# Kernel optimization log

Hardware: AMD Instinct MI355X
Metric: run time of the kernel (lower is better)

Reference implementation:

```python
import jax, jax.numpy as jnp
import numpy as np

B, S, D, H = 2, 2048, 1024, 16
DEPTH = D // H
NEG = -1e9

def setup_inputs() -> dict:
    key = jax.random.key(0)
    k = jax.random.split(key, 4)
    return {
        "token_inputs": jax.random.normal(k[0], (B, S, D), dtype=jnp.float32),
        "mask": jnp.zeros((B, 1, 1, S), dtype=jnp.float32),
        "W_qkv": jax.random.normal(k[1], (D, 3 * D), dtype=jnp.float32) * 0.02,
        "b_qkv": jnp.zeros((3 * D,), dtype=jnp.float32),
        "W_out": jax.random.normal(k[2], (D, D), dtype=jnp.float32) * 0.02,
        "b_out": jnp.zeros((D,), dtype=jnp.float32),
    }

def reference(token_inputs, mask, W_qkv, b_qkv, W_out, b_out):
    # fused QKV projection
    qkv = token_inputs @ W_qkv + b_qkv                       # [B,S,3D]
    q, k, v = jnp.split(qkv, 3, axis=-1)                     # [B,S,D] each
    # split heads -> [B,H,S,depth]
    split = lambda x: x.reshape(B, S, H, DEPTH).transpose(0, 2, 1, 3)
    q, k, v = split(q), split(k), split(v)
    # causal additive mask: 0 on/below diagonal, -1e9 above
    causal = (1.0 - jnp.tril(jnp.ones((S, S), dtype=jnp.float32))) * NEG
    full_mask = mask + causal                                # [B,1,S,S]
    # scaled dot-product attention
    scores = jnp.einsum('bhqd,bhkd->bhqk', q, k) / jnp.sqrt(jnp.float32(DEPTH))
    scores = scores + full_mask
    attn = jax.nn.softmax(scores, axis=-1)                   # [B,H,S,S]
    ctx = jnp.einsum('bhqk,bhkd->bhqd', attn, v)             # [B,H,S,depth]
    # merge heads and final projection
    ctx = ctx.transpose(0, 2, 1, 3).reshape(B, S, D)
    return ctx @ W_out + b_out
```

## Files before the change

kernel.cpp:

```cpp
#include <hip/hip_runtime.h>
#include <hip/hip_bf16.h>

#define B_ 2
#define S_ 2048
#define D_ 1024
#define H_ 16
#define DEPTH_ 64

typedef __attribute__((ext_vector_type(4))) float f32x4;
typedef __attribute__((ext_vector_type(16))) float f32x16;
typedef __attribute__((ext_vector_type(8))) short bf16x8;
typedef const __attribute__((address_space(1))) unsigned int gu32;
typedef __attribute__((address_space(3))) unsigned int lu32;

__device__ __forceinline__ void gload_lds16(const void* g, void* l) {
  __builtin_amdgcn_global_load_lds((gu32*)g, (lu32*)l, 16, 0, 0);
}

__device__ __forceinline__ short f2bf(float f) {
  union { float f; unsigned u; } v; v.f = f;
  return (short)((v.u + 0x7FFFu + ((v.u >> 16) & 1u)) >> 16);
}
__device__ __forceinline__ unsigned pk2(float lo, float hi) {
  unsigned r;
  asm("v_cvt_pk_bf16_f32 %0, %1, %2" : "=v"(r) : "v"(lo), "v"(hi));
  return r;
}

__global__ __launch_bounds__(256) void cast_kernel(const float* __restrict__ in,
                                                   short* __restrict__ out, int n4) {
  int i = blockIdx.x * 256 + threadIdx.x;
  if (i < n4) {
    const float4 v = reinterpret_cast<const float4*>(in)[i];
    short2 a, b;
    *reinterpret_cast<unsigned*>(&a) = pk2(v.x, v.y);
    *reinterpret_cast<unsigned*>(&b) = pk2(v.z, v.w);
    reinterpret_cast<short4*>(out)[i] = make_short4(a.x, a.y, b.x, b.y);
  }
}

__global__ __launch_bounds__(256) void transpose_cast_kernel(const float* __restrict__ W,
                                                             short* __restrict__ WT,
                                                             int K, int N) {
  __shared__ short tile[32][33];
  int n0 = blockIdx.x * 32, k0 = blockIdx.y * 32;
  int tx = threadIdx.x, ty = threadIdx.y;
#pragma unroll
  for (int j = 0; j < 4; ++j)
    tile[ty + 8 * j][tx] = f2bf(W[(size_t)(k0 + ty + 8 * j) * N + n0 + tx]);
  __syncthreads();
#pragma unroll
  for (int j = 0; j < 4; ++j)
    WT[(size_t)(n0 + ty + 8 * j) * K + k0 + tx] = tile[tx][ty + 8 * j];
}

template <int EPI, int BM>
__global__ __launch_bounds__(512) void gemm_bt_kernel(
    const short* __restrict__ A, const short* __restrict__ BT,
    const float* __restrict__ bias,
    short* __restrict__ Qh, short* __restrict__ Kh, short* __restrict__ VTt,
    float* __restrict__ Out, int M, int N, int K) {
  constexpr int MI = BM / 64;
  constexpr int ASZ = BM * 32;
  constexpr int BSZ = 128 * 32;
  __shared__ short smem[2 * ASZ + 2 * BSZ];
  const int bm = blockIdx.y * BM, bn = blockIdx.x * 128;
  const int tid = threadIdx.x;
  const int w = tid >> 6, lane = tid & 63;
  const int wr = w >> 1, wc = w & 1;
  const int lr = lane & 15, lg = lane >> 4;
  const int s_r = lane >> 2, s_c = (lane & 3) * 8;
  f32x4 acc[MI][4] = {};
  const int nk = K >> 5;

  auto stage = [&](int buf, int kt) {
    short* Asb = smem + (buf ? ASZ : 0);
    short* Bsb = smem + 2 * ASZ + (buf ? BSZ : 0);
    if (BM == 128 || w < 4)
      gload_lds16(&A[(size_t)(bm + 16 * w + s_r) * K + kt * 32 + s_c], &Asb[16 * w * 32]);
    gload_lds16(&BT[(size_t)(bn + 16 * w + s_r) * K + kt * 32 + s_c], &Bsb[16 * w * 32]);
  };

  stage(0, 0);
  __syncthreads();
  int cur = 0;
  for (int kt = 0; kt < nk; ++kt) {
    if (kt + 1 < nk) stage(cur ^ 1, kt + 1);
    const short* Asb = smem + (cur ? ASZ : 0);
    const short* Bsb = smem + 2 * ASZ + (cur ? BSZ : 0);
    bf16x8 af[MI], bfr[4];
#pragma unroll
    for (int mi = 0; mi < MI; ++mi)
      af[mi] = *reinterpret_cast<const bf16x8*>(&Asb[((BM / 4) * wr + 16 * mi + lr) * 32 + 8 * lg]);
#pragma unroll
    for (int ni = 0; ni < 4; ++ni)
      bfr[ni] = *reinterpret_cast<const bf16x8*>(&Bsb[(64 * wc + 16 * ni + lr) * 32 + 8 * lg]);
#pragma unroll
    for (int mi = 0; mi < MI; ++mi)
#pragma unroll
      for (int ni = 0; ni < 4; ++ni)
        acc[mi][ni] = __builtin_amdgcn_mfma_f32_16x16x32_bf16(af[mi], bfr[ni], acc[mi][ni], 0, 0, 0);
    __syncthreads();
    cur ^= 1;
  }

  if constexpr (EPI == 0) {
    if (bn >= 2 * D_) {
      __syncthreads();
      short* vt = smem;
#pragma unroll
      for (int mi = 0; mi < MI; ++mi)
#pragma unroll
        for (int ni = 0; ni < 4; ++ni)
#pragma unroll
          for (int r = 0; r < 4; r += 2) {
            int row_local = (BM / 4) * wr + 16 * mi + 4 * lg + r;
            int col_local = 64 * wc + 16 * ni + lr;
            float bv = bias[bn + col_local];
            unsigned u = pk2(acc[mi][ni][r] + bv, acc[mi][ni][r + 1] + bv);
            int rsw = row_local ^ ((col_local & 7) << 3);
            *reinterpret_cast<unsigned*>(&vt[col_local * 128 + rsw]) = u;
          }
      __syncthreads();
      const int b = bm >> 11, sbase = bm & (S_ - 1);
#pragma unroll
      for (int p = 0; p < 4; ++p) {
        int slot = 512 * p + tid;
        int vrow = slot >> 4, seg = slot & 15;
        int dd_col = bn - 2 * D_ + vrow;
        int hh = dd_col >> 6, dd = dd_col & 63;
        int csw = (seg * 8) ^ ((vrow & 7) << 3);
        short* dst = &VTt[((size_t)(b * H_ + hh) * DEPTH_ + dd) * S_ + sbase + seg * 8];
        *reinterpret_cast<bf16x8*>(dst) = *reinterpret_cast<const bf16x8*>(&vt[vrow * 128 + csw]);
      }
    } else {
      constexpr float SCQ = 0.125f * 1.44269504f;
#pragma unroll
      for (int mi = 0; mi < MI; ++mi)
#pragma unroll
        for (int ni = 0; ni < 4; ++ni)
#pragma unroll
          for (int r = 0; r < 4; ++r) {
            int row = bm + (BM / 4) * wr + 16 * mi + 4 * lg + r;
            int col = bn + 64 * wc + 16 * ni + lr;
            float v = acc[mi][ni][r] + bias[col];
            int b = row >> 11, s = row & (S_ - 1);
            int which = col >> 10, cm = col & (D_ - 1);
            int hh = cm >> 6, dd = cm & 63;
            size_t bh = (size_t)(b * H_ + hh);
            if (which == 0) Qh[(bh * S_ + s) * DEPTH_ + dd] = f2bf(v * SCQ);
            else            Kh[(bh * S_ + s) * DEPTH_ + dd] = f2bf(v);
          }
    }
  } else {
#pragma unroll
    for (int mi = 0; mi < MI; ++mi)
#pragma unroll
      for (int ni = 0; ni < 4; ++ni)
#pragma unroll
        for (int r = 0; r < 4; ++r) {
          int row = bm + (BM / 4) * wr + 16 * mi + 4 * lg + r;
          int col = bn + 64 * wc + 16 * ni + lr;
          Out[(size_t)row * N + col] = acc[mi][ni][r] + bias[col];
        }
  }
}

__global__ __launch_bounds__(256, 4) void attn_kernel(
    const short* __restrict__ Qh, const short* __restrict__ Kh,
    const short* __restrict__ VTt, const float* __restrict__ mask,
    short* __restrict__ ctx) {
  constexpr float LOG2E = 1.44269504f;
  __shared__ short smem[16384];
  const int bid = blockIdx.x;
  const int j = bid >> 5, g = j & 7, rr = j >> 3;
  const int qt = (rr == 0) ? 31 - g : (rr == 1) ? 16 + g : (rr == 2) ? 15 - g : g;
  const int bh = bid & 31;
  const int b = bh >> 4, h = bh & 15;
  const short* Qp = Qh + (size_t)bh * S_ * DEPTH_;
  const short* Kp = Kh + (size_t)bh * S_ * DEPTH_;
  const short* Vp = VTt + (size_t)bh * DEPTH_ * S_;
  const int tid = threadIdx.x;
  const int w = tid >> 6, lane = tid & 63;
  const int sw = w & 1, ch = w >> 1;
  const int lq = lane & 31, hi = lane >> 5;
  const int q0w = qt * 64 + sw * 32;
  const int scs = 8 * ((lane & 7) ^ ((lane >> 3) & 7));
  const int srw = lane >> 3;
  short* Ksc = smem + ch * 8192;
  short* Vsc = Ksc + 4096;

  bf16x8 qf[4];
#pragma unroll
  for (int ksd = 0; ksd < 4; ++ksd)
    qf[ksd] = *reinterpret_cast<const bf16x8*>(&Qp[(size_t)(q0w + lq) * DEPTH_ + 16 * ksd + 8 * hi]);

  bf16x8 ones = {};
  if (hi == 0) ones[0] = (short)0x3F80;

  f32x16 acc0 = {}, acc1 = {};
  float l_run = 0.f;

  const int nt = qt + 1;
  const int nh = (nt + 1) >> 1;
  for (int i = 0; i < nh; ++i) {
    const int kt = ch ? (nh + i) : i;
    const bool valid = kt < nt;
    const int k0 = kt * 64;
    __syncthreads();
    if (valid) {
#pragma unroll
      for (int jj = 0; jj < 4; ++jj) {
        const int brow = sw * 32 + jj * 8;
        gload_lds16(&Kp[(size_t)(k0 + brow + srw) * DEPTH_ + scs], &Ksc[brow * 64]);
        gload_lds16(&Vp[(size_t)(brow + srw) * S_ + k0 + scs], &Vsc[brow * 64]);
      }
    }
    __syncthreads();
    if (!valid) continue;

    f32x16 sc[2] = {{}, {}};
#pragma unroll
    for (int h2 = 0; h2 < 2; ++h2) {
#pragma unroll
      for (int ksd = 0; ksd < 4; ++ksd) {
        const int row = h2 * 32 + lq;
        const int col = (16 * ksd + 8 * hi) ^ ((row & 7) * 8);
        bf16x8 kf = *reinterpret_cast<const bf16x8*>(&Ksc[row * 64 + col]);
        sc[h2] = __builtin_amdgcn_mfma_f32_32x32x16_bf16(kf, qf[ksd], sc[h2], 0, 0, 0);
      }
      float mv = mask[(size_t)b * S_ + k0 + h2 * 32 + lq];
      bf16x8 maf = {};
      if (hi == 0) maf[0] = f2bf(LOG2E * mv);
      sc[h2] = __builtin_amdgcn_mfma_f32_32x32x16_bf16(maf, ones, sc[h2], 0, 0, 0);
    }
    if (kt == nt - 1) {
      const int qg = q0w + lq;
#pragma unroll
      for (int h2 = 0; h2 < 2; ++h2)
#pragma unroll
        for (int r = 0; r < 16; ++r) {
          int kvg = k0 + (r & 3) + 8 * (r >> 2) + 4 * hi + 32 * h2;
          if (kvg > qg) sc[h2][r] = -1e30f;
        }
    }
#pragma unroll
    for (int h2 = 0; h2 < 2; ++h2)
#pragma unroll
      for (int r = 0; r < 16; ++r) sc[h2][r] = exp2f(sc[h2][r]);
    float s8[8];
#pragma unroll
    for (int r = 0; r < 8; ++r) s8[r] = (sc[0][r] + sc[0][r + 8]) + (sc[1][r] + sc[1][r + 8]);
#pragma unroll
    for (int r = 0; r < 4; ++r) s8[r] = s8[r] + s8[r + 4];
    float su = (s8[0] + s8[1]) + (s8[2] + s8[3]);
    su += __shfl_xor(su, 32);
    l_run += su;

#pragma unroll
    for (int h2 = 0; h2 < 2; ++h2) {
#pragma unroll
      for (int ks = 0; ks < 2; ++ks) {
        const int rb = 8 * ks;
        unsigned a = pk2(sc[h2][rb + 0], sc[h2][rb + 1]);
        unsigned bq = pk2(sc[h2][rb + 2], sc[h2][rb + 3]);
        unsigned c = pk2(sc[h2][rb + 4], sc[h2][rb + 5]);
        unsigned d = pk2(sc[h2][rb + 6], sc[h2][rb + 7]);
        unsigned sa = __shfl_xor((int)a, 32), sb = __shfl_xor((int)bq, 32);
        unsigned sx = __shfl_xor((int)c, 32), sy = __shfl_xor((int)d, 32);
        union { unsigned u[4]; bf16x8 v; } pf;
        pf.u[0] = hi ? sx : a;
        pf.u[1] = hi ? sy : bq;
        pf.u[2] = hi ? c : sa;
        pf.u[3] = hi ? d : sb;
#pragma unroll
        for (int dh = 0; dh < 2; ++dh) {
          const int row = dh * 32 + lq;
          const int col = (32 * h2 + 16 * ks + 8 * hi) ^ ((row & 7) * 8);
          bf16x8 vf = *reinterpret_cast<const bf16x8*>(&Vsc[row * 64 + col]);
          if (dh == 0) acc0 = __builtin_amdgcn_mfma_f32_32x32x16_bf16(vf, pf.v, acc0, 0, 0, 0);
          else         acc1 = __builtin_amdgcn_mfma_f32_32x32x16_bf16(vf, pf.v, acc1, 0, 0, 0);
        }
      }
    }
  }

  __syncthreads();
  float* F  = (float*)smem;
  float* ML = (float*)(smem + 8192);
  short* ob = smem + 8704;
  if (ch == 1) {
    float* dst = F + ((size_t)sw * 64 + lane) * 32;
#pragma unroll
    for (int r = 0; r < 16; ++r) { dst[r] = acc0[r]; dst[16 + r] = acc1[r]; }
    ML[sw * 64 + lane] = l_run;
  }
  __syncthreads();
  if (ch == 0) {
    const float* src = F + ((size_t)sw * 64 + lane) * 32;
    const float rl = 1.f / (l_run + ML[sw * 64 + lane]);
#pragma unroll
    for (int r = 0; r < 16; ++r) {
      acc0[r] = (acc0[r] + src[r]) * rl;
      acc1[r] = (acc1[r] + src[16 + r]) * rl;
    }
#pragma unroll
    for (int dh = 0; dh < 2; ++dh) {
      const f32x16& Aa = dh ? acc1 : acc0;
#pragma unroll
      for (int gg = 0; gg < 4; ++gg)
#pragma unroll
        for (int p = 0; p < 2; ++p) {
          int r0 = 4 * gg + 2 * p;
          int d0 = 2 * p + 8 * gg + 4 * hi + 32 * dh;
          unsigned u = pk2(Aa[r0], Aa[r0 + 1]);
          *reinterpret_cast<unsigned*>(&ob[(sw * 32 + lq) * 72 + d0]) = u;
        }
    }
  }
  __syncthreads();
  {
    const int row = tid >> 2, seg = tid & 3;
    short* dst = ctx + ((size_t)b * S_ + qt * 64 + row) * D_ + h * 64 + seg * 16;
    const short* srcp = &ob[row * 72 + seg * 16];
    *reinterpret_cast<bf16x8*>(dst) = *reinterpret_cast<const bf16x8*>(srcp);
    *reinterpret_cast<bf16x8*>(dst + 8) = *reinterpret_cast<const bf16x8*>(srcp + 8);
  }
}

extern "C" void kernel_launch(void* const* d_in, const int* in_sizes, int n_in,
                              void* d_out, int out_size, void* d_ws, size_t ws_size,
                              hipStream_t stream) {
  const float* X    = (const float*)d_in[0];
  const float* mask = (const float*)d_in[1];
  const float* Wqkv = (const float*)d_in[2];
  const float* bqkv = (const float*)d_in[3];
  const float* Wout = (const float*)d_in[4];
  const float* bout = (const float*)d_in[5];
  float* Out = (float*)d_out;

  short* ws    = (short*)d_ws;
  short* Xb    = ws;
  short* WqkvT = Xb + (size_t)4096 * 1024;
  short* WoutT = WqkvT + (size_t)3072 * 1024;
  short* Qh    = WoutT + (size_t)1024 * 1024;
  short* Kh    = Qh + (size_t)B_ * H_ * S_ * DEPTH_;
  short* VTt   = Kh + (size_t)B_ * H_ * S_ * DEPTH_;
  short* ctx   = VTt + (size_t)B_ * H_ * S_ * DEPTH_;

  cast_kernel<<<4096, 256, 0, stream>>>(X, Xb, (4096 * 1024) / 4);
  transpose_cast_kernel<<<dim3(96, 32), dim3(32, 8), 0, stream>>>(Wqkv, WqkvT, 1024, 3072);
  transpose_cast_kernel<<<dim3(32, 32), dim3(32, 8), 0, stream>>>(Wout, WoutT, 1024, 1024);
  gemm_bt_kernel<0, 128><<<dim3(24, 32), 512, 0, stream>>>(Xb, WqkvT, bqkv, Qh, Kh, VTt, nullptr,
                                                           4096, 3072, 1024);
  attn_kernel<<<1024, 256, 0, stream>>>(Qh, Kh, VTt, mask, ctx);
  gemm_bt_kernel<1, 64><<<dim3(8, 64), 512, 0, stream>>>(ctx, WoutT, bout, nullptr, nullptr, nullptr,
                                                         Out, 4096, 1024, 1024);
}
```

Before: 115.6 us.

## Register-prefetch K/V tiles in attention and use explicit vmcnt waits in GEMM

After: 164.6 us. 1.42x slower.

```diff
diff --git a/kernel.cpp b/kernel.cpp
--- a/kernel.cpp
+++ b/kernel.cpp
@@ -26,6 +26,13 @@
   asm("v_cvt_pk_bf16_f32 %0, %1, %2" : "=v"(r) : "v"(lo), "v"(hi));
   return r;
 }
+#define BARRIER_RAW() do {                      \
+  __builtin_amdgcn_sched_barrier(0);            \
+  asm volatile("" ::: "memory");                \
+  __builtin_amdgcn_s_barrier();                 \
+  asm volatile("" ::: "memory");                \
+  __builtin_amdgcn_sched_barrier(0);            \
+} while (0)
 
 __global__ __launch_bounds__(256) void cast_kernel(const float* __restrict__ in,
                                                    short* __restrict__ out, int n4) {
@@ -82,10 +89,18 @@
   };
 
   stage(0, 0);
-  __syncthreads();
+  asm volatile("s_waitcnt vmcnt(0)" ::: "memory");
+  BARRIER_RAW();
   int cur = 0;
   for (int kt = 0; kt < nk; ++kt) {
-    if (kt + 1 < nk) stage(cur ^ 1, kt + 1);
+    if (kt + 1 < nk) {
+      stage(cur ^ 1, kt + 1);
+      if (BM == 128 || w < 4) asm volatile("s_waitcnt vmcnt(2)" ::: "memory");
+      else                    asm volatile("s_waitcnt vmcnt(1)" ::: "memory");
+    } else {
+      asm volatile("s_waitcnt vmcnt(0)" ::: "memory");
+    }
+    BARRIER_RAW();
     const short* Asb = smem + (cur ? ASZ : 0);
     const short* Bsb = smem + 2 * ASZ + (cur ? BSZ : 0);
     bf16x8 af[MI], bfr[4];
@@ -100,7 +115,7 @@
 #pragma unroll
       for (int ni = 0; ni < 4; ++ni)
         acc[mi][ni] = __builtin_amdgcn_mfma_f32_16x16x32_bf16(af[mi], bfr[ni], acc[mi][ni], 0, 0, 0);
-    __syncthreads();
+    BARRIER_RAW();
     cur ^= 1;
   }
 
@@ -171,7 +186,8 @@
     const short* __restrict__ VTt, const float* __restrict__ mask,
     short* __restrict__ ctx) {
   constexpr float LOG2E = 1.44269504f;
-  __shared__ short smem[16384];
+  constexpr int LK = 72;
+  __shared__ short smem[2 * 2 * 64 * LK];
   const int bid = blockIdx.x;
   const int j = bid >> 5, g = j & 7, rr = j >> 3;
   const int qt = (rr == 0) ? 31 - g : (rr == 1) ? 16 + g : (rr == 2) ? 15 - g : g;
@@ -185,10 +201,29 @@
   const int sw = w & 1, ch = w >> 1;
   const int lq = lane & 31, hi = lane >> 5;
   const int q0w = qt * 64 + sw * 32;
-  const int scs = 8 * ((lane & 7) ^ ((lane >> 3) & 7));
-  const int srw = lane >> 3;
-  short* Ksc = smem + ch * 8192;
-  short* Vsc = Ksc + 4096;
+  const int lrow = lane >> 3;
+  const int lcol8 = (lane & 7) * 8;
+  short* Ksc = smem + ch * (2 * 64 * LK);
+  short* Vsc = Ksc + 64 * LK;
+
+  bf16x8 tk[4], tv[4];
+  auto loadKV = [&](int kt) {
+    const int k0 = kt * 64;
+#pragma unroll
+    for (int jj = 0; jj < 4; ++jj) {
+      const int row = sw * 32 + jj * 8 + lrow;
+      tk[jj] = *reinterpret_cast<const bf16x8*>(&Kp[(size_t)(k0 + row) * DEPTH_ + lcol8]);
+      tv[jj] = *reinterpret_cast<const bf16x8*>(&Vp[(size_t)row * S_ + k0 + lcol8]);
+    }
+  };
+  auto writeKV = [&]() {
+#pragma unroll
+    for (int jj = 0; jj < 4; ++jj) {
+      const int row = sw * 32 + jj * 8 + lrow;
+      *reinterpret_cast<bf16x8*>(&Ksc[row * LK + lcol8]) = tk[jj];
+      *reinterpret_cast<bf16x8*>(&Vsc[row * LK + lcol8]) = tv[jj];
+    }
+  };
 
   bf16x8 qf[4];
 #pragma unroll
@@ -203,92 +238,90 @@
 
   const int nt = qt + 1;
   const int nh = (nt + 1) >> 1;
+  {
+    const int kt0 = ch ? nh : 0;
+    if (kt0 < nt) { loadKV(kt0); writeKV(); }
+  }
+  __syncthreads();
   for (int i = 0; i < nh; ++i) {
     const int kt = ch ? (nh + i) : i;
     const bool valid = kt < nt;
-    const int k0 = kt * 64;
-    __syncthreads();
+    const bool nvalid = (i + 1 < nh) && (kt + 1 < nt);
+    if (nvalid) loadKV(kt + 1);
     if (valid) {
-#pragma unroll
-      for (int jj = 0; jj < 4; ++jj) {
-        const int brow = sw * 32 + jj * 8;
-        gload_lds16(&Kp[(size_t)(k0 + brow + srw) * DEPTH_ + scs], &Ksc[brow * 64]);
-        gload_lds16(&Vp[(size_t)(brow + srw) * S_ + k0 + scs], &Vsc[brow * 64]);
+      const int k0 = kt * 64;
+      f32x16 sc[2] = {{}, {}};
+#pragma unroll
+      for (int h2 = 0; h2 < 2; ++h2) {
+#pragma unroll
+        for (int ksd = 0; ksd < 4; ++ksd) {
+          const int row = h2 * 32 + lq;
+          bf16x8 kf = *reinterpret_cast<const bf16x8*>(&Ksc[row * LK + 16 * ksd + 8 * hi]);
+          sc[h2] = __builtin_amdgcn_mfma_f32_32x32x16_bf16(kf, qf[ksd], sc[h2], 0, 0, 0);
+        }
+        float mv = mask[(size_t)b * S_ + k0 + h2 * 32 + lq];
+        bf16x8 maf = {};
+        if (hi == 0) maf[0] = f2bf(LOG2E * mv);
+        sc[h2] = __builtin_amdgcn_mfma_f32_32x32x16_bf16(maf, ones, sc[h2], 0, 0, 0);
       }
-    }
-    __syncthreads();
-    if (!valid) continue;
-
-    f32x16 sc[2] = {{}, {}};
-#pragma unroll
-    for (int h2 = 0; h2 < 2; ++h2) {
-#pragma unroll
-      for (int ksd = 0; ksd < 4; ++ksd) {
-        const int row = h2 * 32 + lq;
-        const int col = (16 * ksd + 8 * hi) ^ ((row & 7) * 8);
-        bf16x8 kf = *reinterpret_cast<const bf16x8*>(&Ksc[row * 64 + col]);
-        sc[h2] = __builtin_amdgcn_mfma_f32_32x32x16_bf16(kf, qf[ksd], sc[h2], 0, 0, 0);
+      if (kt == nt - 1) {
+        const int qg = q0w + lq;
+#pragma unroll
+        for (int h2 = 0; h2 < 2; ++h2)
+#pragma unroll
+          for (int r = 0; r < 16; ++r) {
+            int kvg = k0 + (r & 3) + 8 * (r >> 2) + 4 * hi + 32 * h2;
+            if (kvg > qg) sc[h2][r] = -1e30f;
+          }
       }
-      float mv = mask[(size_t)b * S_ + k0 + h2 * 32 + lq];
-      bf16x8 maf = {};
-      if (hi == 0) maf[0] = f2bf(LOG2E * mv);
-      sc[h2] = __builtin_amdgcn_mfma_f32_32x32x16_bf16(maf, ones, sc[h2], 0, 0, 0);
-    }
-    if (kt == nt - 1) {
-      const int qg = q0w + lq;
 #pragma unroll
       for (int h2 = 0; h2 < 2; ++h2)
 #pragma unroll
-        for (int r = 0; r < 16; ++r) {
-          int kvg = k0 + (r & 3) + 8 * (r >> 2) + 4 * hi + 32 * h2;
-          if (kvg > qg) sc[h2][r] = -1e30f;
-        }
-    }
-#pragma unroll
-    for (int h2 = 0; h2 < 2; ++h2)
-#pragma unroll
-      for (int r = 0; r < 16; ++r) sc[h2][r] = exp2f(sc[h2][r]);
-    float s8[8];
-#pragma unroll
-    for (int r = 0; r < 8; ++r) s8[r] = (sc[0][r] + sc[0][r + 8]) + (sc[1][r] + sc[1][r + 8]);
-#pragma unroll
-    for (int r = 0; r < 4; ++r) s8[r] = s8[r] + s8[r + 4];
-    float su = (s8[0] + s8[1]) + (s8[2] + s8[3]);
-    su += __shfl_xor(su, 32);
-    l_run += su;
-
-#pragma unroll
-    for (int h2 = 0; h2 < 2; ++h2) {
-#pragma unroll
-      for (int ks = 0; ks < 2; ++ks) {
-        const int rb = 8 * ks;
-        unsigned a = pk2(sc[h2][rb + 0], sc[h2][rb + 1]);
-        unsigned bq = pk2(sc[h2][rb + 2], sc[h2][rb + 3]);
-        unsigned c = pk2(sc[h2][rb + 4], sc[h2][rb + 5]);
-        unsigned d = pk2(sc[h2][rb + 6], sc[h2][rb + 7]);
-        unsigned sa = __shfl_xor((int)a, 32), sb = __shfl_xor((int)bq, 32);
-        unsigned sx = __shfl_xor((int)c, 32), sy = __shfl_xor((int)d, 32);
-        union { unsigned u[4]; bf16x8 v; } pf;
-        pf.u[0] = hi ? sx : a;
-        pf.u[1] = hi ? sy : bq;
-        pf.u[2] = hi ? c : sa;
-        pf.u[3] = hi ? d : sb;
-#pragma unroll
-        for (int dh = 0; dh < 2; ++dh) {
-          const int row = dh * 32 + lq;
-          const int col = (32 * h2 + 16 * ks + 8 * hi) ^ ((row & 7) * 8);
-          bf16x8 vf = *reinterpret_cast<const bf16x8*>(&Vsc[row * 64 + col]);
-          if (dh == 0) acc0 = __builtin_amdgcn_mfma_f32_32x32x16_bf16(vf, pf.v, acc0, 0, 0, 0);
-          else         acc1 = __builtin_amdgcn_mfma_f32_32x32x16_bf16(vf, pf.v, acc1, 0, 0, 0);
+        for (int r = 0; r < 16; ++r) sc[h2][r] = exp2f(sc[h2][r]);
+      float s8[8];
+#pragma unroll
+      for (int r = 0; r < 8; ++r) s8[r] = (sc[0][r] + sc[0][r + 8]) + (sc[1][r] + sc[1][r + 8]);
+#pragma unroll
+      for (int r = 0; r < 4; ++r) s8[r] = s8[r] + s8[r + 4];
+      float su = (s8[0] + s8[1]) + (s8[2] + s8[3]);
+      su += __shfl_xor(su, 32);
+      l_run += su;
+
+#pragma unroll
+      for (int h2 = 0; h2 < 2; ++h2) {
+#pragma unroll
+        for (int ks = 0; ks < 2; ++ks) {
+          const int rb = 8 * ks;
+          unsigned a = pk2(sc[h2][rb + 0], sc[h2][rb + 1]);
+          unsigned bq = pk2(sc[h2][rb + 2], sc[h2][rb + 3]);
+          unsigned c = pk2(sc[h2][rb + 4], sc[h2][rb + 5]);
+          unsigned d = pk2(sc[h2][rb + 6], sc[h2][rb + 7]);
+          unsigned sa = __shfl_xor((int)a, 32), sb = __shfl_xor((int)bq, 32);
+          unsigned sx = __shfl_xor((int)c, 32), sy = __shfl_xor((int)d, 32);
+          union { unsigned u[4]; bf16x8 v; } pf;
+          pf.u[0] = hi ? sx : a;
+          pf.u[1] = hi ? sy : bq;
+          pf.u[2] = hi ? c : sa;
+          pf.u[3] = hi ? d : sb;
+#pragma unroll
+          for (int dh = 0; dh < 2; ++dh) {
+            const int row = dh * 32 + lq;
+            bf16x8 vf = *reinterpret_cast<const bf16x8*>(
+                &Vsc[row * LK + 32 * h2 + 16 * ks + 8 * hi]);
+            if (dh == 0) acc0 = __builtin_amdgcn_mfma_f32_32x32x16_bf16(vf, pf.v, acc0, 0, 0, 0);
+            else         acc1 = __builtin_amdgcn_mfma_f32_32x32x16_bf16(vf, pf.v, acc1, 0, 0, 0);
+          }
         }
       }
     }
-  }
-
-  __syncthreads();
+    __syncthreads();
+    if (nvalid) writeKV();
+    __syncthreads();
+  }
+
   float* F  = (float*)smem;
   float* ML = (float*)(smem + 8192);
-  short* ob = smem + 8704;
+  short* ob = smem + 8448;
   if (ch == 1) {
     float* dst = F + ((size_t)sw * 64 + lane) * 32;
 #pragma unroll
@@ -299,14 +332,16 @@
   if (ch == 0) {
     const float* src = F + ((size_t)sw * 64 + lane) * 32;
     const float rl = 1.f / (l_run + ML[sw * 64 + lane]);
+    f32x16 o0, o1;
 #pragma unroll
     for (int r = 0; r < 16; ++r) {
-      acc0[r] = (acc0[r] + src[r]) * rl;
-      acc1[r] = (acc1[r] + src[16 + r]) * rl;
-    }
+      o0[r] = (acc0[r] + src[r]) * rl;
+      o1[r] = (acc1[r] + src[16 + r]) * rl;
+    }
+    __syncthreads();
 #pragma unroll
     for (int dh = 0; dh < 2; ++dh) {
-      const f32x16& Aa = dh ? acc1 : acc0;
+      const f32x16& Aa = dh ? o1 : o0;
 #pragma unroll
       for (int gg = 0; gg < 4; ++gg)
 #pragma unroll
@@ -317,6 +352,8 @@
           *reinterpret_cast<unsigned*>(&ob[(sw * 32 + lq) * 72 + d0]) = u;
         }
     }
+  } else {
+    __syncthreads();
   }
   __syncthreads();
   {
```
